# Performance work log

Measured on AMD Instinct MI355X. Metric: run time of the kernel, lower is better.

Reference implementation:

```python
import jax, jax.numpy as jnp
import numpy as np

# Axial permutations for num_dimensions=3, emb_dim=-1 (total rank 5), att_dims=[1,2,3]
PERMS = [[0, 2, 3, 1, 4], [0, 1, 3, 2, 4], [0, 1, 2, 3, 4]]
H_SELF = 8
H_CROSS = 8
E_HEAD = 64  # dims_embed[0] / (num_heads_self + num_heads_cross) = 1024/16


def layernorm(x, eps=1e-5):
    # nn.LayerNorm(elementwise_affine=False)
    m = x.mean(axis=-1, keepdims=True)
    v = x.var(axis=-1, keepdims=True)
    return (x - m) * jax.lax.rsqrt(v + eps)


def cross_attention(x, kv, wq, wkv, h, e):
    # x: [bb, t, d_q], kv: [bb, t_kv, d_kv]
    q = x @ wq                                   # [bb, t, h*e]
    k, v = jnp.split(kv @ wkv, 2, axis=-1)       # each [bb, t_kv, h*e]
    bb, t = q.shape[0], q.shape[1]
    tk = k.shape[1]
    q = q.reshape(bb, t, h, e)
    k = k.reshape(bb, tk, h, e)
    v = v.reshape(bb, tk, h, e)
    dots = jnp.einsum('bihe,bjhe->bhij', q, k) * (e ** -0.5)
    attn = jax.nn.softmax(dots, axis=-1)
    out = jnp.einsum('bhij,bjhe->bihe', attn, v)
    return out.reshape(bb, t, h * e)


def permute_to_from(x, kv, perm, wq, wkv, h, e):
    inv = list(np.argsort(perm))
    ax = jnp.transpose(x, perm)
    axkv = jnp.transpose(kv, perm)
    shape = list(ax.shape)
    shape_kv = list(axkv.shape)
    t, d = shape[-2], shape[-1]
    t_kv, d_kv = shape_kv[-2], shape_kv[-1]
    r1 = shape[1] / shape_kv[1]
    r2 = shape[2] / shape_kv[2]
    if int(r1) != 1:
        axkv = jnp.repeat(axkv, max(1, int(r1)), axis=1)
        ax = jnp.repeat(ax, max(1, int(1.0 / r1)), axis=1)
    if int(r2) != 1:
        axkv = jnp.repeat(axkv, max(1, int(r2)), axis=2)
        ax = jnp.repeat(ax, max(1, int(1.0 / r2)), axis=2)
    assert ax.shape[1:3] == axkv.shape[1:3]
    perm_shape = list(ax.shape)
    out = cross_attention(ax.reshape(-1, t, d), axkv.reshape(-1, t_kv, d_kv), wq, wkv, h, e)
    out = out.reshape(perm_shape[:-1] + [-1])
    if shape[1] < shape_kv[1]:  # field0 coarser along perm dim 1 -> mean-pool back
        out = out.reshape(shape[:2] + [int(1.0 / r1)] + perm_shape[2:-1] + [-1]).mean(axis=2)
    if shape[2] < shape_kv[2]:
        out = out.reshape(shape[:3] + [int(1.0 / r2)] + perm_shape[3:-1] + [-1]).mean(axis=3)
    out = out.reshape(shape[:-1] + [-1])
    return jnp.transpose(out, inv)


def setup_inputs() -> dict:
    key = jax.random.key(0)
    ks = jax.random.split(key, 8)
    B, T, LA, LO, D0, D1 = 32, 12, 12, 12, 1024, 512
    s = 0.02
    return {
        'x0': jax.random.normal(ks[0], (B, T, LA, LO, D0), dtype=jnp.float32),
        'x1': jax.random.normal(ks[1], (B, T, LA // 2, LO // 2, D1), dtype=jnp.float32),
        'wq_self': jax.random.normal(ks[2], (3, D0, 512), dtype=jnp.float32) * s,
        'wkv_self': jax.random.normal(ks[3], (3, D0, 1024), dtype=jnp.float32) * s,
        'wq_cross': jax.random.normal(ks[4], (3, D0, 512), dtype=jnp.float32) * s,
        'wkv_cross': jax.random.normal(ks[5], (3, D1, 1024), dtype=jnp.float32) * s,
        'w_out': jax.random.normal(ks[6], (3, 1024, D0), dtype=jnp.float32) * s,
        'b_out': jnp.zeros((3, D0), dtype=jnp.float32),
    }


def reference(x0, x1, wq_self, wkv_self, wq_cross, wkv_cross, w_out, b_out):
    pass_through = x0
    f0 = layernorm(x0)
    f1 = layernorm(x1)
    for ip, perm in enumerate(PERMS):
        o_self = permute_to_from(f0, f0, perm, wq_self[ip], wkv_self[ip], H_SELF, E_HEAD)
        o_cross = permute_to_from(f0, f1, perm, wq_cross[ip], wkv_cross[ip], H_CROSS, E_HEAD)
        f0 = jnp.concatenate([o_self, o_cross], axis=-1) @ w_out[ip] + b_out[ip]
    return pass_through + f0
```

## Files before the change

kernel.cpp:

```cpp
#include <hip/hip_runtime.h>
#include <hip/hip_bf16.h>


typedef __bf16 bf16x8 __attribute__((ext_vector_type(8)));
typedef float floatx4 __attribute__((ext_vector_type(4)));

#define N0 55296
#define N1 13824

#define RAW_BARRIER() asm volatile("s_barrier" ::: "memory")
#define VMCNT(n) asm volatile("s_waitcnt vmcnt(" #n ")" ::: "memory")

__device__ __forceinline__ void gload16(const void* g, void* l) {
    __builtin_amdgcn_global_load_lds(
        (const __attribute__((address_space(1))) unsigned int*)g,
        (__attribute__((address_space(3))) unsigned int*)l, 16, 0, 0);
}

template <int D>
__device__ __forceinline__ void ln_body(const float* __restrict__ xr,
                                        __hip_bfloat16* __restrict__ yr)
{
    const int tid = threadIdx.x;
    float vals[D / 256];
    float s = 0.f, q = 0.f;
#pragma unroll
    for (int k = 0; k < D / 256; ++k) {
        float v = xr[tid + k * 256];
        vals[k] = v; s += v; q += v * v;
    }
#pragma unroll
    for (int off = 32; off > 0; off >>= 1) {
        s += __shfl_xor(s, off);
        q += __shfl_xor(q, off);
    }
    __shared__ float rs[4], rq[4];
    const int w = tid >> 6;
    if ((tid & 63) == 0) { rs[w] = s; rq[w] = q; }
    __syncthreads();
    s = rs[0] + rs[1] + rs[2] + rs[3];
    q = rq[0] + rq[1] + rq[2] + rq[3];
    const float mean = s * (1.f / D);
    const float var  = q * (1.f / D) - mean * mean;
    const float rstd = rsqrtf(var + 1e-5f);
#pragma unroll
    for (int k = 0; k < D / 256; ++k)
        yr[tid + k * 256] = __float2bfloat16((vals[k] - mean) * rstd);
}

__global__ __launch_bounds__(256)
void ln_all(const float* __restrict__ x0, const float* __restrict__ x1,
            __hip_bfloat16* __restrict__ f0, __hip_bfloat16* __restrict__ f1)
{
    const int row = blockIdx.x;
    if (row < N0) {
        ln_body<1024>(x0 + (size_t)row * 1024, f0 + (size_t)row * 1024);
    } else {
        const int r = row - N0;
        ln_body<512>(x1 + (size_t)r * 512, f1 + (size_t)r * 512);
    }
}

__global__ __launch_bounds__(256)
void transpose_all(const float* __restrict__ wqs, const float* __restrict__ wkvs,
                   const float* __restrict__ wqc, const float* __restrict__ wkvc,
                   const float* __restrict__ wo,
                   __hip_bfloat16* __restrict__ W1t,
                   __hip_bfloat16* __restrict__ W2t,
                   __hip_bfloat16* __restrict__ W3t)
{
    int idx = blockIdx.x;
    const float* src;
    __hip_bfloat16* dst;
    int K, N;
    if (idx < 1536) {
        const int ip = idx / 512; idx %= 512; K = 1024; N = 512;
        src = wqs + (size_t)ip * 524288;  dst = W1t + (size_t)ip * 2097152;
    } else if (idx < 4608) {
        idx -= 1536;
        const int ip = idx / 1024; idx %= 1024; K = 1024; N = 1024;
        src = wkvs + (size_t)ip * 1048576; dst = W1t + (size_t)ip * 2097152 + 524288;
    } else if (idx < 6144) {
        idx -= 4608;
        const int ip = idx / 512; idx %= 512; K = 1024; N = 512;
        src = wqc + (size_t)ip * 524288;  dst = W1t + (size_t)ip * 2097152 + 1572864;
    } else if (idx < 7680) {
        idx -= 6144;
        const int ip = idx / 512; idx %= 512; K = 512; N = 1024;
        src = wkvc + (size_t)ip * 524288; dst = W2t + (size_t)ip * 524288;
    } else {
        idx -= 7680;
        const int ip = idx / 1024; idx %= 1024; K = 1024; N = 1024;
        src = wo + (size_t)ip * 1048576;  dst = W3t + (size_t)ip * 1048576;
    }
    const int tiles_x = N >> 5;
    const int n0 = (idx % tiles_x) * 32, k0 = (idx / tiles_x) * 32;

    __shared__ float tile[32][33];
    const int tx = threadIdx.x & 31, ty = threadIdx.x >> 5;
#pragma unroll
    for (int d = 0; d < 4; ++d)
        tile[ty + d * 8][tx] = src[(size_t)(k0 + ty + d * 8) * N + n0 + tx];
    __syncthreads();
#pragma unroll
    for (int d = 0; d < 4; ++d)
        dst[(size_t)(n0 + ty + d * 8) * K + k0 + tx] = __float2bfloat16(tile[tx][ty + d * 8]);
}

__global__ __launch_bounds__(256)
void cast_w3o(const float* __restrict__ wo, __hip_bfloat16* __restrict__ W3o)
{
    const size_t i = ((size_t)blockIdx.x * 256 + threadIdx.x) * 4;
    const float4 v = *(const float4*)(wo + i);
    __hip_bfloat16 o[4] = { __float2bfloat16(v.x), __float2bfloat16(v.y),
                            __float2bfloat16(v.z), __float2bfloat16(v.w) };
    *(uint2*)(W3o + i) = *(const uint2*)o;
}

__global__ __launch_bounds__(256)
void bfold_kernel(const float* __restrict__ b_out,
                  const __hip_bfloat16* __restrict__ W1t,
                  float* __restrict__ bf)
{
    const int idx = blockIdx.x * 256 + threadIdx.x;
    const int j = idx >> 11, n = idx & 2047;
    const float* b = b_out + j * 1024;
    const __hip_bfloat16* w = W1t + ((size_t)(j + 1) * 2048 + n) * 1024;
    float s = 0.f;
#pragma unroll 4
    for (int d = 0; d < 1024; ++d) s += b[d] * __bfloat162float(w[d]);
    bf[idx] = s;
}

template <int EPI>
__global__ __launch_bounds__(512)
void gemm8p(const __hip_bfloat16* __restrict__ A,
            const __hip_bfloat16* __restrict__ Bt,
            void* __restrict__ Cv,
            const float* __restrict__ bias,
            const float* __restrict__ resid,
            int M, int N, int K, int lda)
{
    __shared__ __align__(16) char lds[131072];

    const int gx  = gridDim.x;
    const int nwg = gx * gridDim.y;
    const int bid = blockIdx.y * gx + blockIdx.x;
    const int swz = (bid & 7) * (nwg >> 3) + (bid >> 3);
    const int m0 = (swz / gx) * 256;
    const int n0 = (swz % gx) * 256;

    const int t    = threadIdx.x;
    const int w    = t >> 6;
    const int lane = t & 63;
    const int wr   = w >> 2;
    const int wc   = w & 3;
    const int fr   = lane & 15;
    const int ksl  = lane >> 4;

    floatx4 acc[8][4] = {};

    const int tr   = t >> 3;
    const int scol = ((t & 7) ^ (tr & 7)) << 3;
    const __hip_bfloat16* aG = A  + (size_t)(m0 + tr) * lda + scol;
    const __hip_bfloat16* bG = Bt + (size_t)(n0 + ((tr >> 5) * 64) + (tr & 31)) * K + scol;
    const int ldst = t * 16;

    const int cg0 = ksl ^ (fr & 7);
    const int aO0 = (wr * 64 + fr) * 128 + cg0 * 16;
    const int bO0 = (wc * 32 + fr) * 128 + cg0 * 16;

    auto stageA = [&](char* buf, int h, int ka) {
        gload16(aG + ka + (size_t)(h * 64)       * lda, buf + h * 16384 + ldst);
        gload16(aG + ka + (size_t)(h * 64 + 128) * lda, buf + h * 16384 + 8192 + ldst);
    };
    auto stageB = [&](char* buf, int h, int kb) {
        gload16(bG + kb + (size_t)(h * 32)       * K, buf + 32768 + h * 16384 + ldst);
        gload16(bG + kb + (size_t)(h * 32 + 128) * K, buf + 32768 + h * 16384 + 8192 + ldst);
    };

    const char* bufC = lds;
    auto ldA = [&](int h, bf16x8 (&a)[2][4]) {
#pragma unroll
        for (int mm = 0; mm < 4; ++mm) {
            a[0][mm] = *(const bf16x8*)(bufC + h * 16384 + mm * 2048 + aO0);
            a[1][mm] = *(const bf16x8*)(bufC + h * 16384 + mm * 2048 + (aO0 ^ 64));
        }
    };
    auto ldB = [&](int h, bf16x8 (&b)[2][2]) {
#pragma unroll
        for (int nn = 0; nn < 2; ++nn) {
            b[0][nn] = *(const bf16x8*)(bufC + 32768 + h * 16384 + nn * 2048 + bO0);
            b[1][nn] = *(const bf16x8*)(bufC + 32768 + h * 16384 + nn * 2048 + (bO0 ^ 64));
        }
    };
    auto quad = [&](bf16x8 (&a)[2][4], bf16x8 (&b)[2][2], int mlo, int nlo) {
        __builtin_amdgcn_s_setprio(1);
#pragma unroll
        for (int kk = 0; kk < 2; ++kk)
#pragma unroll
            for (int mm = 0; mm < 4; ++mm)
#pragma unroll
                for (int nn = 0; nn < 2; ++nn)
                    acc[mlo + mm][nlo + nn] = __builtin_amdgcn_mfma_f32_16x16x32_bf16(
                        a[kk][mm], b[kk][nn], acc[mlo + mm][nlo + nn], 0, 0, 0);
        __builtin_amdgcn_s_setprio(0);
    };

    const int NT = K >> 6;

    stageA(lds, 0, 0);
    stageB(lds, 0, 0);
    stageA(lds, 1, 0);
    stageB(lds, 1, 0);
    VMCNT(4);
    RAW_BARRIER();

    bf16x8 a0[2][4], a1[2][4], b0[2][2], b1[2][2];

    for (int tt = 0; tt < NT - 1; ++tt) {
        bufC = lds + ((tt & 1) << 16);
        char* bufN = lds + (((tt + 1) & 1) << 16);
        const int kc = (tt + 1) << 6;
        ldA(0, a0); ldB(0, b0);
        stageA(bufN, 0, kc);
        RAW_BARRIER(); __builtin_amdgcn_sched_barrier(0);
        quad(a0, b0, 0, 0);
        VMCNT(4); RAW_BARRIER();
        ldA(1, a1);
        stageB(bufN, 0, kc);
        RAW_BARRIER(); __builtin_amdgcn_sched_barrier(0);
        quad(a1, b0, 4, 0);
        VMCNT(4); RAW_BARRIER();
        ldB(1, b1);
        stageA(bufN, 1, kc);
        RAW_BARRIER(); __builtin_amdgcn_sched_barrier(0);
        quad(a0, b1, 0, 2);
        RAW_BARRIER();
        stageB(bufN, 1, kc);
        RAW_BARRIER(); __builtin_amdgcn_sched_barrier(0);
        quad(a1, b1, 4, 2);
        VMCNT(4); RAW_BARRIER();
    }

    bufC = lds + (((NT - 1) & 1) << 16);
    ldA(0, a0); ldB(0, b0);
    RAW_BARRIER(); __builtin_amdgcn_sched_barrier(0);
    quad(a0, b0, 0, 0);
    VMCNT(2); RAW_BARRIER();
    ldA(1, a1);
    RAW_BARRIER(); __builtin_amdgcn_sched_barrier(0);
    quad(a1, b0, 4, 0);
    VMCNT(0); RAW_BARRIER();
    ldB(1, b1);
    RAW_BARRIER(); __builtin_amdgcn_sched_barrier(0);
    quad(a0, b1, 0, 2);
    quad(a1, b1, 4, 2);

#pragma unroll
    for (int m = 0; m < 8; ++m) {
#pragma unroll
        for (int n = 0; n < 4; ++n) {
            const int col = n0 + wc * 64 + n * 16 + fr;
#pragma unroll
            for (int r = 0; r < 4; ++r) {
                const int row = m0 + wr * 128 + m * 16 + ksl * 4 + r;
                const size_t idx = (size_t)row * N + col;
                const float v = acc[m][n][r];
                if (EPI == 0) {
                    ((__hip_bfloat16*)Cv)[idx] = __float2bfloat16(v);
                } else if (EPI == 1) {
                    ((__hip_bfloat16*)Cv)[idx] = __float2bfloat16(v + bias[col]);
                } else {
                    ((float*)Cv)[idx] = resid[idx] + v + bias[col];
                }
            }
        }
    }
}

__global__ __launch_bounds__(256)
void attn_kernel(const __hip_bfloat16* __restrict__ qkv,
                 const __hip_bfloat16* __restrict__ kvc, int ldkv,
                 __hip_bfloat16* __restrict__ oc, int ldo, int cross_off,
                 int ip)
{
    __shared__ __align__(16) __hip_bfloat16 Qs[12][520];
    __shared__ __align__(16) __hip_bfloat16 Ks[12][520];
    __shared__ __align__(16) __hip_bfloat16 Vs[12][520];
    __shared__ float P[8][12][12];

    const int g = blockIdx.x;
    const bool cross = blockIdx.y != 0;
    const int tid = threadIdx.x;

    const int b  = g / 144;
    const int r1 = (g % 144) / 12;
    const int r2 = g % 12;
    int n_base, qstride, kvb, kvstride, tk;
    if (ip == 0) {
        n_base = b * 1728 + r1 * 12 + r2; qstride = 144;
        kvb = b * 432 + (r1 >> 1) * 6 + (r2 >> 1); kvstride = 36; tk = 12;
    } else if (ip == 1) {
        n_base = b * 1728 + r1 * 144 + r2; qstride = 12;
        kvb = b * 432 + r1 * 36 + (r2 >> 1); kvstride = 6; tk = 6;
    } else {
        n_base = b * 1728 + r1 * 144 + r2 * 12; qstride = 1;
        kvb = b * 432 + r1 * 36 + (r2 >> 1) * 6; kvstride = 1; tk = 6;
    }
    if (!cross) tk = 12;

    const int qoff = cross ? 1536 : 0;
    for (int idx = tid; idx < 12 * 64; idx += 256) {
        const int i = idx >> 6, c = idx & 63;
        const uint4* src = (const uint4*)(qkv + (size_t)(n_base + i * qstride) * 2048 + qoff);
        *(uint4*)(&Qs[i][c * 8]) = src[c];
    }
    if (!cross) {
        for (int idx = tid; idx < 12 * 64; idx += 256) {
            const int j = idx >> 6, c = idx & 63;
            const __hip_bfloat16* row = qkv + (size_t)(n_base + j * qstride) * 2048;
            *(uint4*)(&Ks[j][c * 8]) = ((const uint4*)(row + 512))[c];
            *(uint4*)(&Vs[j][c * 8]) = ((const uint4*)(row + 1024))[c];
        }
    } else {
        for (int idx = tid; idx < tk * 64; idx += 256) {
            const int j = idx >> 6, c = idx & 63;
            const __hip_bfloat16* row = kvc + (size_t)(kvb + j * kvstride) * ldkv;
            *(uint4*)(&Ks[j][c * 8]) = ((const uint4*)(row))[c];
            *(uint4*)(&Vs[j][c * 8]) = ((const uint4*)(row + 512))[c];
        }
    }
    __syncthreads();

    const int ndots = 8 * 12 * tk;
    for (int idx = tid; idx < ndots; idx += 256) {
        const int h = idx / (12 * tk);
        const int rem = idx % (12 * tk);
        const int i = rem / tk, j = rem % tk;
        const __hip_bfloat162* q2 = (const __hip_bfloat162*)(&Qs[i][h * 64]);
        const __hip_bfloat162* k2 = (const __hip_bfloat162*)(&Ks[j][h * 64]);
        float s = 0.f;
#pragma unroll
        for (int e = 0; e < 32; ++e) {
            const float2 qf = __bfloat1622float2(q2[e]);
            const float2 kf = __bfloat1622float2(k2[e]);
            s += qf.x * kf.x + qf.y * kf.y;
        }
        P[h][i][j] = s * 0.125f;
    }
    __syncthreads();

    if (tid < 96) {
        const int h = tid / 12, i = tid % 12;
        float mx = -1e30f;
        for (int j = 0; j < tk; ++j) mx = fmaxf(mx, P[h][i][j]);
        float sum = 0.f;
        for (int j = 0; j < tk; ++j) { const float e = __expf(P[h][i][j] - mx); P[h][i][j] = e; sum += e; }
        const float inv = 1.f / sum;
        for (int j = 0; j < tk; ++j) P[h][i][j] *= inv;
    }
    __syncthreads();

    for (int idx = tid; idx < 12 * 512; idx += 256) {
        const int i = idx >> 9, c = idx & 511;
        const int h = c >> 6;
        float a = 0.f;
        for (int j = 0; j < tk; ++j)
            a += P[h][i][j] * __bfloat162float(Vs[j][c]);
        oc[(size_t)(n_base + i * qstride) * ldo + (cross ? cross_off : 0) + c] = __float2bfloat16(a);
    }
}

extern "C" void kernel_launch(void* const* d_in, const int* in_sizes, int n_in,
                              void* d_out, int out_size, void* d_ws, size_t ws_size,
                              hipStream_t stream)
{
    (void)in_sizes; (void)n_in; (void)out_size; (void)ws_size;
    const float* x0        = (const float*)d_in[0];
    const float* x1        = (const float*)d_in[1];
    const float* wq_self   = (const float*)d_in[2];
    const float* wkv_self  = (const float*)d_in[3];
    const float* wq_cross  = (const float*)d_in[4];
    const float* wkv_cross = (const float*)d_in[5];
    const float* w_out     = (const float*)d_in[6];
    const float* b_out     = (const float*)d_in[7];

    __hip_bfloat16* qkv = (__hip_bfloat16*)d_out;

    char* ws = (char*)d_ws;
    size_t off = 0;
    auto alloc = [&](size_t bytes) {
        void* p = ws + off;
        off += (bytes + 255) & ~(size_t)255;
        return p;
    };
    __hip_bfloat16* f0   = (__hip_bfloat16*)alloc((size_t)N0 * 1024 * 2);
    __hip_bfloat16* f1   = (__hip_bfloat16*)alloc((size_t)N1 * 512 * 2);
    __hip_bfloat16* kvc3 = (__hip_bfloat16*)alloc((size_t)N1 * 3072 * 2);
    __hip_bfloat16* W1t  = (__hip_bfloat16*)alloc((size_t)3 * 2048 * 1024 * 2);
    __hip_bfloat16* W2t  = (__hip_bfloat16*)alloc((size_t)3 * 1024 * 512 * 2);
    __hip_bfloat16* W3t  = (__hip_bfloat16*)alloc((size_t)3 * 1024 * 1024 * 2);
    __hip_bfloat16* W3o  = (__hip_bfloat16*)alloc((size_t)2 * 1024 * 1024 * 2);
    __hip_bfloat16* Wf   = (__hip_bfloat16*)alloc((size_t)2 * 2048 * 1024 * 2);
    float*          bfo  = (float*)alloc((size_t)2 * 2048 * 4);

    ln_all<<<N0 + N1, 256, 0, stream>>>(x0, x1, f0, f1);
    transpose_all<<<10752, 256, 0, stream>>>(wq_self, wkv_self, wq_cross,
                                             wkv_cross, w_out, W1t, W2t, W3t);
    cast_w3o<<<2048, 256, 0, stream>>>(w_out, W3o);
    bfold_kernel<<<16, 256, 0, stream>>>(b_out, W1t, bfo);
    for (int j = 0; j < 2; ++j)
        gemm8p<0><<<dim3(4, 8), 512, 0, stream>>>(
            W1t + (size_t)(j + 1) * 2048 * 1024, W3o + (size_t)j * 1024 * 1024,
            Wf + (size_t)j * 2048 * 1024, nullptr, nullptr, 2048, 1024, 1024, 1024);
    gemm8p<0><<<dim3(12, 54), 512, 0, stream>>>(
        f1, W2t, kvc3, nullptr, nullptr, N1, 3072, 512, 512);

    for (int ip = 0; ip < 3; ++ip) {
        if (ip == 0) {
            gemm8p<0><<<dim3(8, 216), 512, 0, stream>>>(
                f0, W1t, qkv, nullptr, nullptr, N0, 2048, 1024, 1024);
        } else {
            gemm8p<1><<<dim3(8, 216), 512, 0, stream>>>(
                f0, Wf + (size_t)(ip - 1) * 2048 * 1024, qkv,
                bfo + (ip - 1) * 2048, nullptr, N0, 2048, 1024, 1024);
        }
        attn_kernel<<<dim3(4608, 2), 256, 0, stream>>>(
            qkv, kvc3 + ip * 1024, 3072, f0, 1024, 512, ip);
    }
    gemm8p<2><<<dim3(4, 216), 512, 0, stream>>>(
        f0, W3t + (size_t)2 * 1024 * 1024, d_out, b_out + 2 * 1024, x0,
        N0, 1024, 1024, 1024);
}
```

Measured before the change: 1.740 ms.

## Gather permuted rows in GEMM A-load and fuse self/cross attention into one kernel

The QKV GEMM now gathers its A rows through a permutation map, so each attention axis sequence lands in 12 contiguous rows of the qkv buffer. The attention kernel can then read one contiguous 12x2048 block and write its output contiguously. Self and cross attention are merged into a single 512-thread block per sequence, and the probability buffer is stored in bf16. In exchange, the GEMM A loads become row gathers, f0 is kept in a rotated layout across stages, and storing probabilities in bf16 slightly reduces precision.

Result: faster. 1.597 ms (-8.2%).

```diff
diff --git a/kernel.cpp b/kernel.cpp
--- a/kernel.cpp
+++ b/kernel.cpp
@@ -15,6 +15,16 @@
     __builtin_amdgcn_global_load_lds(
         (const __attribute__((address_space(1))) unsigned int*)g,
         (__attribute__((address_space(3))) unsigned int*)l, 16, 0, 0);
+}
+
+template <int SIG>
+__device__ __forceinline__ int mapRow(int i) {
+    if (SIG == 0) return i;
+    const int b = i / 1728, r = i % 1728;
+    const int d1 = r / 144, r2 = r % 144, d2 = r2 / 12, d3 = r2 % 12;
+    if (SIG == 1) return b * 1728 + d3 * 144 + d1 * 12 + d2;
+    if (SIG == 2) return b * 1728 + d3 * 144 + d2 * 12 + d1;
+    return b * 1728 + d1 * 144 + d3 * 12 + d2;
 }
 
 template <int D>
@@ -132,7 +142,7 @@
     bf[idx] = s;
 }
 
-template <int EPI>
+template <int EPI, int SIG>
 __global__ __launch_bounds__(512)
 void gemm8p(const __hip_bfloat16* __restrict__ A,
             const __hip_bfloat16* __restrict__ Bt,
@@ -162,7 +172,10 @@
 
     const int tr   = t >> 3;
     const int scol = ((t & 7) ^ (tr & 7)) << 3;
-    const __hip_bfloat16* aG = A  + (size_t)(m0 + tr) * lda + scol;
+    const __hip_bfloat16* aP[4];
+#pragma unroll
+    for (int r = 0; r < 4; ++r)
+        aP[r] = A + (size_t)mapRow<SIG>(m0 + tr + r * 64) * lda + scol;
     const __hip_bfloat16* bG = Bt + (size_t)(n0 + ((tr >> 5) * 64) + (tr & 31)) * K + scol;
     const int ldst = t * 16;
 
@@ -171,8 +184,8 @@
     const int bO0 = (wc * 32 + fr) * 128 + cg0 * 16;
 
     auto stageA = [&](char* buf, int h, int ka) {
-        gload16(aG + ka + (size_t)(h * 64)       * lda, buf + h * 16384 + ldst);
-        gload16(aG + ka + (size_t)(h * 64 + 128) * lda, buf + h * 16384 + 8192 + ldst);
+        gload16(aP[h]     + ka, buf + h * 16384 + ldst);
+        gload16(aP[h + 2] + ka, buf + h * 16384 + 8192 + ldst);
     };
     auto stageB = [&](char* buf, int h, int kb) {
         gload16(bG + kb + (size_t)(h * 32)       * K, buf + 32768 + h * 16384 + ldst);
@@ -279,67 +292,58 @@
     }
 }
 
-__global__ __launch_bounds__(256)
-void attn_kernel(const __hip_bfloat16* __restrict__ qkv,
-                 const __hip_bfloat16* __restrict__ kvc, int ldkv,
-                 __hip_bfloat16* __restrict__ oc, int ldo, int cross_off,
-                 int ip)
-{
-    __shared__ __align__(16) __hip_bfloat16 Qs[12][520];
-    __shared__ __align__(16) __hip_bfloat16 Ks[12][520];
-    __shared__ __align__(16) __hip_bfloat16 Vs[12][520];
-    __shared__ float P[8][12][12];
-
-    const int g = blockIdx.x;
-    const bool cross = blockIdx.y != 0;
+__global__ __launch_bounds__(512)
+void attn_fused(const __hip_bfloat16* __restrict__ qkv,
+                const __hip_bfloat16* __restrict__ kvc,
+                __hip_bfloat16* __restrict__ out, int ip)
+{
+    __shared__ __align__(16) __hip_bfloat16 R[12][2052];
+    __shared__ __align__(16) __hip_bfloat16 KV[12][1032];
+    __shared__ __hip_bfloat16 P[16][12][12];
+
+    const int g   = blockIdx.x;
     const int tid = threadIdx.x;
 
     const int b  = g / 144;
-    const int r1 = (g % 144) / 12;
-    const int r2 = g % 12;
-    int n_base, qstride, kvb, kvstride, tk;
+    const int u1 = (g / 12) % 12;
+    const int u2 = g % 12;
+    int kvb, kvstride, tkc;
     if (ip == 0) {
-        n_base = b * 1728 + r1 * 12 + r2; qstride = 144;
-        kvb = b * 432 + (r1 >> 1) * 6 + (r2 >> 1); kvstride = 36; tk = 12;
+        kvb = b * 432 + (u1 >> 1) * 6 + (u2 >> 1); kvstride = 36; tkc = 12;
     } else if (ip == 1) {
-        n_base = b * 1728 + r1 * 144 + r2; qstride = 12;
-        kvb = b * 432 + r1 * 36 + (r2 >> 1); kvstride = 6; tk = 6;
+        kvb = b * 432 + u1 * 36 + (u2 >> 1); kvstride = 6; tkc = 6;
     } else {
-        n_base = b * 1728 + r1 * 144 + r2 * 12; qstride = 1;
-        kvb = b * 432 + r1 * 36 + (r2 >> 1) * 6; kvstride = 1; tk = 6;
-    }
-    if (!cross) tk = 12;
-
-    const int qoff = cross ? 1536 : 0;
-    for (int idx = tid; idx < 12 * 64; idx += 256) {
-        const int i = idx >> 6, c = idx & 63;
-        const uint4* src = (const uint4*)(qkv + (size_t)(n_base + i * qstride) * 2048 + qoff);
-        *(uint4*)(&Qs[i][c * 8]) = src[c];
-    }
-    if (!cross) {
-        for (int idx = tid; idx < 12 * 64; idx += 256) {
-            const int j = idx >> 6, c = idx & 63;
-            const __hip_bfloat16* row = qkv + (size_t)(n_base + j * qstride) * 2048;
-            *(uint4*)(&Ks[j][c * 8]) = ((const uint4*)(row + 512))[c];
-            *(uint4*)(&Vs[j][c * 8]) = ((const uint4*)(row + 1024))[c];
-        }
-    } else {
-        for (int idx = tid; idx < tk * 64; idx += 256) {
-            const int j = idx >> 6, c = idx & 63;
-            const __hip_bfloat16* row = kvc + (size_t)(kvb + j * kvstride) * ldkv;
-            *(uint4*)(&Ks[j][c * 8]) = ((const uint4*)(row))[c];
-            *(uint4*)(&Vs[j][c * 8]) = ((const uint4*)(row + 512))[c];
-        }
+        kvb = b * 432 + u1 * 36 + (u2 >> 1) * 6; kvstride = 1; tkc = 6;
+    }
+
+    const uint4* src = (const uint4*)(qkv + (size_t)g * 12 * 2048);
+    for (int idx = tid; idx < 12 * 256; idx += 512) {
+        const int row = idx >> 8, cg = idx & 255;
+        *(uint4*)(&R[row][cg * 8]) = src[row * 256 + cg];
+    }
+    for (int idx = tid; idx < tkc * 128; idx += 512) {
+        const int row = idx >> 7, cg = idx & 127;
+        const uint4* kvr = (const uint4*)(kvc + (size_t)(kvb + row * kvstride) * 3072);
+        *(uint4*)(&KV[row][cg * 8]) = kvr[cg];
     }
     __syncthreads();
 
-    const int ndots = 8 * 12 * tk;
-    for (int idx = tid; idx < ndots; idx += 256) {
-        const int h = idx / (12 * tk);
-        const int rem = idx % (12 * tk);
-        const int i = rem / tk, j = rem % tk;
-        const __hip_bfloat162* q2 = (const __hip_bfloat162*)(&Qs[i][h * 64]);
-        const __hip_bfloat162* k2 = (const __hip_bfloat162*)(&Ks[j][h * 64]);
+    const int nd_self = 8 * 12 * 12;
+    const int nd = nd_self + 8 * 12 * tkc;
+    for (int idx = tid; idx < nd; idx += 512) {
+        int h, i, j;
+        const __hip_bfloat162 *q2, *k2;
+        bool self = idx < nd_self;
+        if (self) {
+            h = idx / 144; const int rem = idx % 144; i = rem / 12; j = rem % 12;
+            q2 = (const __hip_bfloat162*)(&R[i][h * 64]);
+            k2 = (const __hip_bfloat162*)(&R[j][512 + h * 64]);
+        } else {
+            const int x = idx - nd_self;
+            h = x / (12 * tkc); const int rem = x % (12 * tkc); i = rem / tkc; j = rem % tkc;
+            q2 = (const __hip_bfloat162*)(&R[i][1536 + h * 64]);
+            k2 = (const __hip_bfloat162*)(&KV[j][h * 64]);
+        }
         float s = 0.f;
 #pragma unroll
         for (int e = 0; e < 32; ++e) {
@@ -347,28 +351,46 @@
             const float2 kf = __bfloat1622float2(k2[e]);
             s += qf.x * kf.x + qf.y * kf.y;
         }
-        P[h][i][j] = s * 0.125f;
+        P[self ? h : 8 + h][i][j] = __float2bfloat16(s * 0.125f);
     }
     __syncthreads();
 
-    if (tid < 96) {
-        const int h = tid / 12, i = tid % 12;
+    if (tid < 192) {
+        const int half = tid / 96, h = (tid % 96) / 12, i = tid % 12;
+        const int tk = half ? tkc : 12;
+        __hip_bfloat16* p = &P[half * 8 + h][i][0];
+        float v[12];
         float mx = -1e30f;
-        for (int j = 0; j < tk; ++j) mx = fmaxf(mx, P[h][i][j]);
+        for (int j = 0; j < tk; ++j) { v[j] = __bfloat162float(p[j]); mx = fmaxf(mx, v[j]); }
         float sum = 0.f;
-        for (int j = 0; j < tk; ++j) { const float e = __expf(P[h][i][j] - mx); P[h][i][j] = e; sum += e; }
+        for (int j = 0; j < tk; ++j) { v[j] = __expf(v[j] - mx); sum += v[j]; }
         const float inv = 1.f / sum;
-        for (int j = 0; j < tk; ++j) P[h][i][j] *= inv;
+        for (int j = 0; j < tk; ++j) p[j] = __float2bfloat16(v[j] * inv);
     }
     __syncthreads();
 
-    for (int idx = tid; idx < 12 * 512; idx += 256) {
-        const int i = idx >> 9, c = idx & 511;
-        const int h = c >> 6;
-        float a = 0.f;
-        for (int j = 0; j < tk; ++j)
-            a += P[h][i][j] * __bfloat162float(Vs[j][c]);
-        oc[(size_t)(n_base + i * qstride) * ldo + (cross ? cross_off : 0) + c] = __float2bfloat16(a);
+    for (int idx = tid; idx < 12 * 512; idx += 512) {
+        const int i = idx >> 9, c2 = idx & 511;
+        const int col = c2 * 2;
+        float a0 = 0.f, a1 = 0.f;
+        if (c2 < 256) {
+            const int h = col >> 6;
+            for (int j = 0; j < 12; ++j) {
+                const float p = __bfloat162float(P[h][i][j]);
+                a0 += p * __bfloat162float(R[j][1024 + col]);
+                a1 += p * __bfloat162float(R[j][1024 + col + 1]);
+            }
+        } else {
+            const int cc = col - 512;
+            const int h = cc >> 6;
+            for (int j = 0; j < tkc; ++j) {
+                const float p = __bfloat162float(P[8 + h][i][j]);
+                a0 += p * __bfloat162float(KV[j][512 + cc]);
+                a1 += p * __bfloat162float(KV[j][512 + cc + 1]);
+            }
+        }
+        __hip_bfloat16 o[2] = { __float2bfloat16(a0), __float2bfloat16(a1) };
+        *(uint*)(out + (size_t)(g * 12 + i) * 1024 + col) = *(const uint*)o;
     }
 }
 
@@ -411,25 +433,25 @@
     cast_w3o<<<2048, 256, 0, stream>>>(w_out, W3o);
     bfold_kernel<<<16, 256, 0, stream>>>(b_out, W1t, bfo);
     for (int j = 0; j < 2; ++j)
-        gemm8p<0><<<dim3(4, 8), 512, 0, stream>>>(
+        gemm8p<0, 0><<<dim3(4, 8), 512, 0, stream>>>(
             W1t + (size_t)(j + 1) * 2048 * 1024, W3o + (size_t)j * 1024 * 1024,
             Wf + (size_t)j * 2048 * 1024, nullptr, nullptr, 2048, 1024, 1024, 1024);
-    gemm8p<0><<<dim3(12, 54), 512, 0, stream>>>(
+    gemm8p<0, 0><<<dim3(12, 54), 512, 0, stream>>>(
         f1, W2t, kvc3, nullptr, nullptr, N1, 3072, 512, 512);
 
-    for (int ip = 0; ip < 3; ++ip) {
-        if (ip == 0) {
-            gemm8p<0><<<dim3(8, 216), 512, 0, stream>>>(
-                f0, W1t, qkv, nullptr, nullptr, N0, 2048, 1024, 1024);
-        } else {
-            gemm8p<1><<<dim3(8, 216), 512, 0, stream>>>(
-                f0, Wf + (size_t)(ip - 1) * 2048 * 1024, qkv,
-                bfo + (ip - 1) * 2048, nullptr, N0, 2048, 1024, 1024);
-        }
-        attn_kernel<<<dim3(4608, 2), 256, 0, stream>>>(
-            qkv, kvc3 + ip * 1024, 3072, f0, 1024, 512, ip);
-    }
-    gemm8p<2><<<dim3(4, 216), 512, 0, stream>>>(
+    gemm8p<0, 1><<<dim3(8, 216), 512, 0, stream>>>(
+        f0, W1t, qkv, nullptr, nullptr, N0, 2048, 1024, 1024);
+    attn_fused<<<4608, 512, 0, stream>>>(qkv, kvc3, f0, 0);
+
+    gemm8p<1, 2><<<dim3(8, 216), 512, 0, stream>>>(
+        f0, Wf, qkv, bfo, nullptr, N0, 2048, 1024, 1024);
+    attn_fused<<<4608, 512, 0, stream>>>(qkv, kvc3 + 1024, f0, 1);
+
+    gemm8p<1, 3><<<dim3(8, 216), 512, 0, stream>>>(
+        f0, Wf + (size_t)2048 * 1024, qkv, bfo + 2048, nullptr, N0, 2048, 1024, 1024);
+    attn_fused<<<4608, 512, 0, stream>>>(qkv, kvc3 + 2048, f0, 2);
+
+    gemm8p<2, 0><<<dim3(4, 216), 512, 0, stream>>>(
         f0, W3t + (size_t)2 * 1024 * 1024, d_out, b_out + 2 * 1024, x0,
         N0, 1024, 1024, 1024);
 }
```
